# Optimization experiments

Hardware: AMD Instinct MI355X
Metric: run time of the kernel (lower is better)

The kernel has to match this reference:

```python
import jax, jax.numpy as jnp
import numpy as np

D_MODEL = 4096
N_HEADS = 32
HEAD_DIM = 128
MAX_SEQ = 512


def setup_inputs() -> dict:
    key = jax.random.key(0)
    ks = jax.random.split(key, 14)
    w_scale = 1.0 / np.sqrt(D_MODEL)
    inp = {
        "query": jax.random.normal(ks[0], (1, 1, D_MODEL), jnp.float32),
        "key_value_source": jax.random.normal(ks[1], (1, 1, D_MODEL), jnp.float32),
        "step": jax.random.randint(ks[2], (1,), 0, MAX_SEQ, jnp.int32),
        "key_buffer": jax.random.normal(ks[3], (1, N_HEADS, MAX_SEQ, HEAD_DIM), jnp.float32),
        "value_buffer": jax.random.normal(ks[4], (1, N_HEADS, MAX_SEQ, HEAD_DIM), jnp.float32),
        "Wq": jax.random.normal(ks[5], (D_MODEL, D_MODEL), jnp.float32) * w_scale,
        "bq": jax.random.normal(ks[6], (D_MODEL,), jnp.float32) * 0.01,
        "Wk": jax.random.normal(ks[7], (D_MODEL, D_MODEL), jnp.float32) * w_scale,
        "bk": jax.random.normal(ks[8], (D_MODEL,), jnp.float32) * 0.01,
        "Wv": jax.random.normal(ks[9], (D_MODEL, D_MODEL), jnp.float32) * w_scale,
        "bv": jax.random.normal(ks[10], (D_MODEL,), jnp.float32) * 0.01,
        "Wo": jax.random.normal(ks[11], (D_MODEL, D_MODEL), jnp.float32) * w_scale,
        "bo": jax.random.normal(ks[12], (D_MODEL,), jnp.float32) * 0.01,
    }
    return inp


def reference(query, key_value_source, step, key_buffer, value_buffer,
              Wq, bq, Wk, bk, Wv, bv, Wo, bo):
    # q/k/v projections on the single new token: [1,1,D] -> [1,H,1,HD]
    q = (query @ Wq.T + bq).reshape(1, 1, N_HEADS, HEAD_DIM).transpose(0, 2, 1, 3)
    k_new = (key_value_source @ Wk.T + bk).reshape(1, 1, N_HEADS, HEAD_DIM).transpose(0, 2, 1, 3)
    v_new = (key_value_source @ Wv.T + bv).reshape(1, 1, N_HEADS, HEAD_DIM).transpose(0, 2, 1, 3)

    positions = jnp.arange(MAX_SEQ)                       # [S]
    write_mask = (positions == step)[None, None, :, None]  # [1,1,S,1]
    key_buffer = jnp.where(write_mask, k_new, key_buffer)     # scatter-write at step
    value_buffer = jnp.where(write_mask, v_new, value_buffer)

    scale = 1.0 / np.sqrt(HEAD_DIM)
    attn_mask = jnp.where(positions <= step, 0.0, -jnp.inf)[None, None, None, :]  # [1,1,1,S]
    scores = jnp.einsum("bhqd,bhsd->bhqs", q, key_buffer) * scale + attn_mask
    weights = jax.nn.softmax(scores, axis=-1)
    attn_out = jnp.einsum("bhqs,bhsd->bhqd", weights, value_buffer)  # [1,H,1,HD]

    attn_out = attn_out.transpose(0, 2, 1, 3).reshape(1, 1, D_MODEL)
    output = attn_out @ Wo.T + bo
    return output, key_buffer, value_buffer
```

## Files before the change

kernel.cpp:

```cpp
#include <hip/hip_runtime.h>

#define D_MODEL 4096
#define N_HEADS 32
#define HEAD_DIM 128
#define MAX_SEQ 512
#define SPLITS 8
#define SPLIT_LEN (MAX_SEQ / SPLITS)

__global__ __launch_bounds__(256) void qkv_gemv(
        const float* __restrict__ Wq, const float* __restrict__ bq,
        const float* __restrict__ Wk, const float* __restrict__ bk,
        const float* __restrict__ Wv, const float* __restrict__ bv,
        const float* __restrict__ query, const float* __restrict__ kvsrc,
        const int* __restrict__ step_p,
        float* __restrict__ qkv_out,
        float* __restrict__ out_kb, float* __restrict__ out_vb) {
    const int wid  = (blockIdx.x * blockDim.x + threadIdx.x) >> 6;
    const int lane = threadIdx.x & 63;
    const int r0   = wid << 1;
    const int which = r0 >> 12;
    const int row   = r0 & (D_MODEL - 1);

    const float* W = (which == 0) ? Wq : (which == 1) ? Wk : Wv;
    const float* b = (which == 0) ? bq : (which == 1) ? bk : bv;
    const float* x = (which == 0) ? query : kvsrc;

    const float4* A = (const float4*)(W + (size_t)row * D_MODEL);
    const float4* B = A + D_MODEL / 4;
    const float4* X = (const float4*)x;

    float4 a0 = A[lane],      b0 = B[lane],      x0 = X[lane];
    float4 a1 = A[64 + lane], b1 = B[64 + lane], x1 = X[64 + lane];
    float acc0 = 0.f, acc1 = 0.f;
#pragma unroll
    for (int j = 0; j < 16; ++j) {
        float4 ac = a0, bc = b0, xc = x0;
        a0 = a1; b0 = b1; x0 = x1;
        if (j < 14) {
            const int o = (j + 2) * 64 + lane;
            a1 = A[o]; b1 = B[o]; x1 = X[o];
        }
        acc0 += ac.x * xc.x + ac.y * xc.y + ac.z * xc.z + ac.w * xc.w;
        acc1 += bc.x * xc.x + bc.y * xc.y + bc.z * xc.z + bc.w * xc.w;
    }
#pragma unroll
    for (int off = 32; off > 0; off >>= 1) {
        acc0 += __shfl_xor(acc0, off);
        acc1 += __shfl_xor(acc1, off);
    }
    if (lane == 0) {
        const float v0 = acc0 + b[row];
        const float v1 = acc1 + b[row + 1];
        qkv_out[r0]     = v0;
        qkv_out[r0 + 1] = v1;
        if (which != 0) {
            const int step = *step_p;
            float* dst = (which == 1) ? out_kb : out_vb;
            const int h0 = row >> 7, d0 = row & (HEAD_DIM - 1);
            dst[((size_t)h0 * MAX_SEQ + step) * HEAD_DIM + d0]     = v0;
            const int r1 = row + 1;
            dst[((size_t)(r1 >> 7) * MAX_SEQ + step) * HEAD_DIM + (r1 & (HEAD_DIM - 1))] = v1;
        }
    }
}

__global__ void kv_update(const float4* __restrict__ kb, const float4* __restrict__ vb,
                          const int* __restrict__ step_p,
                          float4* __restrict__ out_kb, float4* __restrict__ out_vb) {
    const int step = *step_p;
    int i = blockIdx.x * blockDim.x + threadIdx.x;
#pragma unroll
    for (int t = 0; t < 2; ++t, i += 1024 * 256) {
        const int s = (i >> 5) & (MAX_SEQ - 1);
        if (s != step) {
            out_kb[i] = kb[i];
            out_vb[i] = vb[i];
        }
    }
}

__global__ void attn_split(const float* __restrict__ q,
                           const float* __restrict__ kb,
                           const float* __restrict__ vb,
                           const int* __restrict__ step_p,
                           float* __restrict__ pm, float* __restrict__ pl,
                           float* __restrict__ po) {
    const int bid = blockIdx.x;
    const int h   = bid >> 3;
    const int sp  = bid & (SPLITS - 1);
    const int tid = threadIdx.x;
    const int n   = *step_p + 1;
    const int s0  = sp * SPLIT_LEN;
    const int cnt = min(SPLIT_LEN, n - s0);

    if (cnt <= 0) {
        if (tid == 0) { pm[bid] = -1e30f; pl[bid] = 0.f; }
        if (tid < HEAD_DIM) po[bid * HEAD_DIM + tid] = 0.f;
        return;
    }

    __shared__ float sq[HEAD_DIM];
    __shared__ float w[SPLIT_LEN];
    __shared__ float pv[2][HEAD_DIM];

    if (tid < HEAD_DIM) sq[tid] = q[h * HEAD_DIM + tid];
    __syncthreads();

    {
        const int p = tid >> 2;
        const int g = tid & 3;
        float acc = 0.f;
        if (p < cnt) {
            const float4* krow = (const float4*)(kb + ((size_t)(h * MAX_SEQ + s0 + p)) * HEAD_DIM);
            const float4* q4   = (const float4*)sq;
#pragma unroll
            for (int j = 0; j < 8; ++j) {
                float4 kk = krow[g * 8 + j];
                float4 qq = q4[g * 8 + j];
                acc += kk.x * qq.x + kk.y * qq.y + kk.z * qq.z + kk.w * qq.w;
            }
        }
        acc += __shfl_xor(acc, 1);
        acc += __shfl_xor(acc, 2);
        if ((g == 0) && (p < cnt)) w[p] = acc * 0.08838834764831845f;
    }
    __syncthreads();

    if (tid < 64) {
        float mv = (tid < cnt) ? w[tid] : -1e30f;
#pragma unroll
        for (int off = 32; off > 0; off >>= 1) mv = fmaxf(mv, __shfl_xor(mv, off));
        float e = (tid < cnt) ? __expf(w[tid] - mv) : 0.f;
        if (tid < cnt) w[tid] = e;
        float sum = e;
#pragma unroll
        for (int off = 32; off > 0; off >>= 1) sum += __shfl_xor(sum, off);
        if (tid == 0) { pm[bid] = mv; pl[bid] = sum; }
    }
    __syncthreads();

    const int d    = tid & (HEAD_DIM - 1);
    const int half = tid >> 7;
    float acc = 0.f;
    for (int s = half; s < cnt; s += 2)
        acc += w[s] * vb[((size_t)(h * MAX_SEQ + s0 + s)) * HEAD_DIM + d];
    pv[half][d] = acc;
    __syncthreads();
    if (tid < HEAD_DIM)
        po[bid * HEAD_DIM + tid] = pv[0][tid] + pv[1][tid];
}

__global__ void attn_combine(const float* __restrict__ pm, const float* __restrict__ pl,
                             const float* __restrict__ po, float* __restrict__ attn_out) {
    const int h = blockIdx.x;
    const int d = threadIdx.x;
    float m = -1e30f;
#pragma unroll
    for (int j = 0; j < SPLITS; ++j) m = fmaxf(m, pm[h * SPLITS + j]);
    float l = 0.f, o = 0.f;
#pragma unroll
    for (int j = 0; j < SPLITS; ++j) {
        float sc = __expf(pm[h * SPLITS + j] - m);
        l += pl[h * SPLITS + j] * sc;
        o += po[(h * SPLITS + j) * HEAD_DIM + d] * sc;
    }
    attn_out[h * HEAD_DIM + d] = o / l;
}

__global__ __launch_bounds__(256) void out_gemv(const float* __restrict__ Wo,
                                                const float* __restrict__ bo,
                                                const float* __restrict__ x,
                                                float* __restrict__ out) {
    __shared__ float r[4];
    const int wv   = threadIdx.x >> 6;
    const int lane = threadIdx.x & 63;
    const int row  = (blockIdx.x << 1) + (wv >> 1);
    const int half = wv & 1;

    const float4* A = (const float4*)(Wo + (size_t)row * D_MODEL) + (half << 9);
    const float4* X = (const float4*)x + (half << 9);

    float4 a0 = A[lane], x0 = X[lane];
    float4 a1 = A[64 + lane], x1 = X[64 + lane];
    float acc = 0.f;
#pragma unroll
    for (int j = 0; j < 8; ++j) {
        float4 ac = a0, xc = x0;
        a0 = a1; x0 = x1;
        if (j < 6) {
            const int o = (j + 2) * 64 + lane;
            a1 = A[o]; x1 = X[o];
        }
        acc += ac.x * xc.x + ac.y * xc.y + ac.z * xc.z + ac.w * xc.w;
    }
#pragma unroll
    for (int off = 32; off > 0; off >>= 1) acc += __shfl_xor(acc, off);
    if (lane == 0) r[wv] = acc;
    __syncthreads();
    if (threadIdx.x < 2) {
        const int rr = (blockIdx.x << 1) + threadIdx.x;
        out[rr] = r[threadIdx.x * 2] + r[threadIdx.x * 2 + 1] + bo[rr];
    }
}

extern "C" void kernel_launch(void* const* d_in, const int* in_sizes, int n_in,
                              void* d_out, int out_size, void* d_ws, size_t ws_size,
                              hipStream_t stream) {
    const float* query  = (const float*)d_in[0];
    const float* kvsrc  = (const float*)d_in[1];
    const int*   step_p = (const int*)d_in[2];
    const float* kb     = (const float*)d_in[3];
    const float* vb     = (const float*)d_in[4];
    const float* Wq     = (const float*)d_in[5];
    const float* bq     = (const float*)d_in[6];
    const float* Wk     = (const float*)d_in[7];
    const float* bk     = (const float*)d_in[8];
    const float* Wv     = (const float*)d_in[9];
    const float* bv     = (const float*)d_in[10];
    const float* Wo     = (const float*)d_in[11];
    const float* bo     = (const float*)d_in[12];

    float* out    = (float*)d_out;
    float* out_kb = out + D_MODEL;
    float* out_vb = out_kb + N_HEADS * MAX_SEQ * HEAD_DIM;

    float* qkv  = (float*)d_ws;
    float* qv   = qkv;
    float* attn = qkv + 3 * D_MODEL;
    float* pm   = attn + D_MODEL;
    float* pl   = pm + N_HEADS * SPLITS;
    float* po   = pl + N_HEADS * SPLITS;

    qkv_gemv<<<1536, 256, 0, stream>>>(Wq, bq, Wk, bk, Wv, bv, query, kvsrc,
                                       step_p, qkv, out_kb, out_vb);

    kv_update<<<1024, 256, 0, stream>>>((const float4*)kb, (const float4*)vb,
                                        step_p, (float4*)out_kb, (float4*)out_vb);

    attn_split<<<N_HEADS * SPLITS, 256, 0, stream>>>(qv, out_kb, out_vb, step_p, pm, pl, po);
    attn_combine<<<N_HEADS, HEAD_DIM, 0, stream>>>(pm, pl, po, attn);

    out_gemv<<<2048, 256, 0, stream>>>(Wo, bo, attn, out);
}
```

Measured before the change: 69.96 us.

## Fuse KV-cache copy into QKV projection kernel and stage x in LDS

Merges the KV-buffer copy kernel into the QKV GEMV launch by interleaving copy blocks (every fourth block) with projection blocks, removing one kernel launch and letting the copy traffic overlap with weight streaming. Both GEMV kernels now assign one full row per wavefront, stage the input vector in shared memory, and issue all 16 float4 weight loads up front instead of using a two-deep software pipeline. The out-projection no longer does a cross-wave shared-memory reduction. The trade-off is higher register use for the 16 preloaded float4 values, plus a redundant 16KB shared-memory fill per block.

```diff
diff --git a/kernel.cpp b/kernel.cpp
--- a/kernel.cpp
+++ b/kernel.cpp
@@ -7,74 +7,73 @@
 #define SPLITS 8
 #define SPLIT_LEN (MAX_SEQ / SPLITS)
 
-__global__ __launch_bounds__(256) void qkv_gemv(
+__global__ __launch_bounds__(256) void proj_copy(
         const float* __restrict__ Wq, const float* __restrict__ bq,
         const float* __restrict__ Wk, const float* __restrict__ bk,
         const float* __restrict__ Wv, const float* __restrict__ bv,
         const float* __restrict__ query, const float* __restrict__ kvsrc,
         const int* __restrict__ step_p,
+        const float4* __restrict__ kb, const float4* __restrict__ vb,
         float* __restrict__ qkv_out,
         float* __restrict__ out_kb, float* __restrict__ out_vb) {
-    const int wid  = (blockIdx.x * blockDim.x + threadIdx.x) >> 6;
+    const int bid = blockIdx.x;
+
+    if ((bid & 3) == 3) {
+        const int step = *step_p;
+        int i = (bid >> 2) * 256 + threadIdx.x;
+#pragma unroll
+        for (int t = 0; t < 2; ++t, i += 1024 * 256) {
+            const int s = (i >> 5) & (MAX_SEQ - 1);
+            if (s != step) {
+                ((float4*)out_kb)[i] = kb[i];
+                ((float4*)out_vb)[i] = vb[i];
+            }
+        }
+        return;
+    }
+
+    const int gid  = (bid >> 2) * 3 + (bid & 3);
+    const int wv   = threadIdx.x >> 6;
     const int lane = threadIdx.x & 63;
-    const int r0   = wid << 1;
-    const int which = r0 >> 12;
-    const int row   = r0 & (D_MODEL - 1);
+    const int r    = gid * 4 + wv;
+    const int which = r >> 12;
+    const int row   = r & (D_MODEL - 1);
+
+    const float* x = (which == 0) ? query : kvsrc;
+
+    __shared__ float4 xs[D_MODEL / 4];
+    {
+        const float4* X = (const float4*)x;
+#pragma unroll
+        for (int t = 0; t < 4; ++t)
+            xs[threadIdx.x + 256 * t] = X[threadIdx.x + 256 * t];
+    }
+    __syncthreads();
 
     const float* W = (which == 0) ? Wq : (which == 1) ? Wk : Wv;
     const float* b = (which == 0) ? bq : (which == 1) ? bk : bv;
-    const float* x = (which == 0) ? query : kvsrc;
-
     const float4* A = (const float4*)(W + (size_t)row * D_MODEL);
-    const float4* B = A + D_MODEL / 4;
-    const float4* X = (const float4*)x;
-
-    float4 a0 = A[lane],      b0 = B[lane],      x0 = X[lane];
-    float4 a1 = A[64 + lane], b1 = B[64 + lane], x1 = X[64 + lane];
-    float acc0 = 0.f, acc1 = 0.f;
-#pragma unroll
-    for (int j = 0; j < 16; ++j) {
-        float4 ac = a0, bc = b0, xc = x0;
-        a0 = a1; b0 = b1; x0 = x1;
-        if (j < 14) {
-            const int o = (j + 2) * 64 + lane;
-            a1 = A[o]; b1 = B[o]; x1 = X[o];
-        }
-        acc0 += ac.x * xc.x + ac.y * xc.y + ac.z * xc.z + ac.w * xc.w;
-        acc1 += bc.x * xc.x + bc.y * xc.y + bc.z * xc.z + bc.w * xc.w;
-    }
-#pragma unroll
-    for (int off = 32; off > 0; off >>= 1) {
-        acc0 += __shfl_xor(acc0, off);
-        acc1 += __shfl_xor(acc1, off);
-    }
+
+    float4 a[16];
+#pragma unroll
+    for (int i = 0; i < 16; ++i) a[i] = A[i * 64 + lane];
+
+    float acc = 0.f;
+#pragma unroll
+    for (int i = 0; i < 16; ++i) {
+        const float4 xv = xs[i * 64 + lane];
+        acc += a[i].x * xv.x + a[i].y * xv.y + a[i].z * xv.z + a[i].w * xv.w;
+    }
+#pragma unroll
+    for (int off = 32; off > 0; off >>= 1) acc += __shfl_xor(acc, off);
+
     if (lane == 0) {
-        const float v0 = acc0 + b[row];
-        const float v1 = acc1 + b[row + 1];
-        qkv_out[r0]     = v0;
-        qkv_out[r0 + 1] = v1;
+        const float v = acc + b[row];
+        qkv_out[r] = v;
         if (which != 0) {
             const int step = *step_p;
             float* dst = (which == 1) ? out_kb : out_vb;
-            const int h0 = row >> 7, d0 = row & (HEAD_DIM - 1);
-            dst[((size_t)h0 * MAX_SEQ + step) * HEAD_DIM + d0]     = v0;
-            const int r1 = row + 1;
-            dst[((size_t)(r1 >> 7) * MAX_SEQ + step) * HEAD_DIM + (r1 & (HEAD_DIM - 1))] = v1;
-        }
-    }
-}
-
-__global__ void kv_update(const float4* __restrict__ kb, const float4* __restrict__ vb,
-                          const int* __restrict__ step_p,
-                          float4* __restrict__ out_kb, float4* __restrict__ out_vb) {
-    const int step = *step_p;
-    int i = blockIdx.x * blockDim.x + threadIdx.x;
-#pragma unroll
-    for (int t = 0; t < 2; ++t, i += 1024 * 256) {
-        const int s = (i >> 5) & (MAX_SEQ - 1);
-        if (s != step) {
-            out_kb[i] = kb[i];
-            out_vb[i] = vb[i];
+            dst[((size_t)(row >> 7) * MAX_SEQ + step) * HEAD_DIM + (row & (HEAD_DIM - 1))] = v;
         }
     }
 }
@@ -171,36 +170,33 @@
                                                 const float* __restrict__ bo,
                                                 const float* __restrict__ x,
                                                 float* __restrict__ out) {
-    __shared__ float r[4];
     const int wv   = threadIdx.x >> 6;
     const int lane = threadIdx.x & 63;
-    const int row  = (blockIdx.x << 1) + (wv >> 1);
-    const int half = wv & 1;
-
-    const float4* A = (const float4*)(Wo + (size_t)row * D_MODEL) + (half << 9);
-    const float4* X = (const float4*)x + (half << 9);
-
-    float4 a0 = A[lane], x0 = X[lane];
-    float4 a1 = A[64 + lane], x1 = X[64 + lane];
+    const int row  = blockIdx.x * 4 + wv;
+
+    __shared__ float4 xs[D_MODEL / 4];
+    {
+        const float4* X = (const float4*)x;
+#pragma unroll
+        for (int t = 0; t < 4; ++t)
+            xs[threadIdx.x + 256 * t] = X[threadIdx.x + 256 * t];
+    }
+    __syncthreads();
+
+    const float4* A = (const float4*)(Wo + (size_t)row * D_MODEL);
+    float4 a[16];
+#pragma unroll
+    for (int i = 0; i < 16; ++i) a[i] = A[i * 64 + lane];
+
     float acc = 0.f;
 #pragma unroll
-    for (int j = 0; j < 8; ++j) {
-        float4 ac = a0, xc = x0;
-        a0 = a1; x0 = x1;
-        if (j < 6) {
-            const int o = (j + 2) * 64 + lane;
-            a1 = A[o]; x1 = X[o];
-        }
-        acc += ac.x * xc.x + ac.y * xc.y + ac.z * xc.z + ac.w * xc.w;
+    for (int i = 0; i < 16; ++i) {
+        const float4 xv = xs[i * 64 + lane];
+        acc += a[i].x * xv.x + a[i].y * xv.y + a[i].z * xv.z + a[i].w * xv.w;
     }
 #pragma unroll
     for (int off = 32; off > 0; off >>= 1) acc += __shfl_xor(acc, off);
-    if (lane == 0) r[wv] = acc;
-    __syncthreads();
-    if (threadIdx.x < 2) {
-        const int rr = (blockIdx.x << 1) + threadIdx.x;
-        out[rr] = r[threadIdx.x * 2] + r[threadIdx.x * 2 + 1] + bo[rr];
-    }
+    if (lane == 0) out[row] = acc + bo[row];
 }
 
 extern "C" void kernel_launch(void* const* d_in, const int* in_sizes, int n_in,
@@ -231,14 +227,12 @@
     float* pl   = pm + N_HEADS * SPLITS;
     float* po   = pl + N_HEADS * SPLITS;
 
-    qkv_gemv<<<1536, 256, 0, stream>>>(Wq, bq, Wk, bk, Wv, bv, query, kvsrc,
-                                       step_p, qkv, out_kb, out_vb);
-
-    kv_update<<<1024, 256, 0, stream>>>((const float4*)kb, (const float4*)vb,
-                                        step_p, (float4*)out_kb, (float4*)out_vb);
+    proj_copy<<<4096, 256, 0, stream>>>(Wq, bq, Wk, bk, Wv, bv, query, kvsrc,
+                                        step_p, (const float4*)kb, (const float4*)vb,
+                                        qkv, out_kb, out_vb);
 
     attn_split<<<N_HEADS * SPLITS, 256, 0, stream>>>(qv, out_kb, out_vb, step_p, pm, pl, po);
     attn_combine<<<N_HEADS, HEAD_DIM, 0, stream>>>(pm, pl, po, attn);
 
-    out_gemv<<<2048, 256, 0, stream>>>(Wo, bo, attn, out);
-}
+    out_gemv<<<1024, 256, 0, stream>>>(Wo, bo, attn, out);
+}
```

Result: slower. 72.32 us (+3.4%).
